# Kernel tuning notes

Hardware: AMD Instinct MI355X
Metric: run time of the kernel (lower is better)

The kernel has to match this reference:

```python
import jax, jax.numpy as jnp
import numpy as np

N, E, G = 50000, 1600000, 512
IN, HID, PROJ = 128, 128, 256


def setup_inputs() -> dict:
    key = jax.random.key(0)
    ks = jax.random.split(key, 20)
    s = 0.05
    return {
        'x1': jax.random.normal(ks[0], (N, IN), jnp.float32),
        'edge_index1': jax.random.randint(ks[1], (2, E), 0, N),
        'batch1': jnp.sort(jax.random.randint(ks[2], (N,), 0, G)),
        'x2': jax.random.normal(ks[3], (N, IN), jnp.float32),
        'edge_index2': jax.random.randint(ks[4], (2, E), 0, N),
        'batch2': jnp.sort(jax.random.randint(ks[5], (N,), 0, G)),
        'W1': jax.random.normal(ks[6], (IN, HID), jnp.float32) * s,
        'b1': jnp.zeros((HID,), jnp.float32),
        'W2': jax.random.normal(ks[7], (HID, HID), jnp.float32) * s,
        'b2': jnp.zeros((HID,), jnp.float32),
        'W3': jax.random.normal(ks[8], (HID, HID), jnp.float32) * s,
        'b3': jnp.zeros((HID,), jnp.float32),
        'Wp1': jax.random.normal(ks[9], (HID, PROJ), jnp.float32) * s,
        'bp1': jnp.zeros((PROJ,), jnp.float32),
        'gamma1': jnp.ones((PROJ,), jnp.float32),
        'beta1': jnp.zeros((PROJ,), jnp.float32),
        'Wp2': jax.random.normal(ks[10], (PROJ, PROJ), jnp.float32) * s,
        'bp2': jnp.zeros((PROJ,), jnp.float32),
        'gamma2': jnp.ones((PROJ,), jnp.float32),
        'beta2': jnp.zeros((PROJ,), jnp.float32),
        'Wq1': jax.random.normal(ks[11], (PROJ, PROJ // 2), jnp.float32) * s,
        'bq1': jnp.zeros((PROJ // 2,), jnp.float32),
        'Wq2': jax.random.normal(ks[12], (PROJ // 2, PROJ), jnp.float32) * s,
        'bq2': jnp.zeros((PROJ,), jnp.float32),
    }


def _gcn_conv(x, src, dst, W, b):
    # PyG GCNConv: add self-loops, symmetric norm, gather -> scatter-add
    n = x.shape[0]
    h = x @ W                                   # [n, out]
    loop = jnp.arange(n)
    s = jnp.concatenate([src, loop])
    d = jnp.concatenate([dst, loop])
    deg = jax.ops.segment_sum(jnp.ones(s.shape[0], h.dtype), d, num_segments=n)
    dinv = jnp.where(deg > 0, 1.0 / jnp.sqrt(deg), 0.0)
    norm = (dinv[s] * dinv[d])[:, None]         # [E+n, 1]
    out = jax.ops.segment_sum(h[s] * norm, d, num_segments=n)
    return out + b


def _encode(x, edge_index, batch, W1, b1, W2, b2, W3, b3):
    src, dst = edge_index[0], edge_index[1]
    h = jax.nn.relu(_gcn_conv(x, src, dst, W1, b1))
    h = jax.nn.relu(_gcn_conv(h, src, dst, W2, b2)) + h
    h = jax.nn.relu(_gcn_conv(h, src, dst, W3, b3)) + h
    # global mean pool over graph ids
    s = jax.ops.segment_sum(h, batch, num_segments=G)
    cnt = jax.ops.segment_sum(jnp.ones(h.shape[0], h.dtype), batch, num_segments=G)
    return s / jnp.maximum(cnt, 1.0)[:, None]


def _batchnorm(x, gamma, beta):
    m = x.mean(axis=0)
    v = x.var(axis=0)  # biased, matches torch BN normalization
    return gamma * (x - m) / jnp.sqrt(v + 1e-5) + beta


def _projector(h, Wp1, bp1, g1, be1, Wp2, bp2, g2, be2):
    z = jax.nn.relu(_batchnorm(h @ Wp1 + bp1, g1, be1))
    return _batchnorm(z @ Wp2 + bp2, g2, be2)


def _predictor(z, Wq1, bq1, Wq2, bq2):
    return jax.nn.relu(z @ Wq1 + bq1) @ Wq2 + bq2


def reference(x1, edge_index1, batch1, x2, edge_index2, batch2,
              W1, b1, W2, b2, W3, b3,
              Wp1, bp1, gamma1, beta1, Wp2, bp2, gamma2, beta2,
              Wq1, bq1, Wq2, bq2):
    h1 = _encode(x1, edge_index1, batch1, W1, b1, W2, b2, W3, b3)
    h2 = _encode(x2, edge_index2, batch2, W1, b1, W2, b2, W3, b3)
    z1 = _projector(h1, Wp1, bp1, gamma1, beta1, Wp2, bp2, gamma2, beta2)
    z2 = _projector(h2, Wp1, bp1, gamma1, beta1, Wp2, bp2, gamma2, beta2)
    p1 = _predictor(z1, Wq1, bq1, Wq2, bq2)
    p2 = _predictor(z2, Wq1, bq1, Wq2, bq2)
    return (p1, p2, z1, z2)
```

## Files before the change

### kernel.cpp

```cpp
#include <hip/hip_runtime.h>
#include <hip/hip_bf16.h>

#define NN     50000
#define NN2    100000
#define NEDGE  1600000
#define NE2    3200000
#define NG     512
#define FIN    128
#define FHID   128
#define FPROJ  256

#define BSH    9
#define BSZ    512
#define NBUCK  98
#define NBUCK2 196
#define EPB    8192
#define NABLK  196
#define NABLK2 392
#define NHIST2 (NBUCK2*NABLK2)
#define NSB1   ((NHIST2 + 255) / 256)

typedef __attribute__((ext_vector_type(8))) short short8;
typedef __attribute__((ext_vector_type(4))) float f32x4;

static __device__ __forceinline__ short f2bf(float f) {
    union { float f; unsigned u; } x; x.f = f;
    unsigned r = (x.u + 0x7FFFu + ((x.u >> 16) & 1u)) >> 16;
    return (short)(r & 0xFFFFu);
}
static __device__ __forceinline__ float bf2f(unsigned short u) {
    union { unsigned u; float f; } x; x.u = ((unsigned)u) << 16;
    return x.f;
}
static __device__ __forceinline__ float bflo(unsigned u) {
    union { unsigned u; float f; } x; x.u = u << 16; return x.f;
}
static __device__ __forceinline__ float bfhi(unsigned u) {
    union { unsigned u; float f; } x; x.u = u & 0xFFFF0000u; return x.f;
}
static __device__ __forceinline__ unsigned packbf(float a, float b) {
    return (unsigned)(unsigned short)f2bf(a) | ((unsigned)(unsigned short)f2bf(b) << 16);
}


__global__ __launch_bounds__(1024) void k_bhist(const int* __restrict__ dst0,
                                                const int* __restrict__ dst1,
                                                int* __restrict__ histG,
                                                unsigned short* __restrict__ lrank) {
    __shared__ int h[NBUCK2];
    for (int j = threadIdx.x; j < NBUCK2; j += 1024) h[j] = 0;
    __syncthreads();
    int b = blockIdx.x;
    int g = b / NABLK, blk = b % NABLK;
    const int* dst = g ? dst1 : dst0;
    int base = blk * EPB;
    int gb = g * NBUCK;
    for (int t = threadIdx.x; t < EPB; t += 1024) {
        int i = base + t;
        if (i < NEDGE)
            lrank[(size_t)g * NEDGE + i] =
                (unsigned short)atomicAdd(&h[gb + (dst[i] >> BSH)], 1);
    }
    __syncthreads();
    for (int j = threadIdx.x; j < NBUCK2; j += 1024)
        histG[(size_t)j * NABLK2 + b] = h[j];
}

__global__ void s_scan256(const int* __restrict__ in, int* __restrict__ out,
                          int* __restrict__ bsum, int n) {
    __shared__ int s[256];
    int i = blockIdx.x * 256 + threadIdx.x;
    int v = (i < n) ? in[i] : 0;
    s[threadIdx.x] = v;
    for (int o = 1; o < 256; o <<= 1) {
        __syncthreads();
        int t = (threadIdx.x >= o) ? s[threadIdx.x - o] : 0;
        __syncthreads();
        s[threadIdx.x] += t;
    }
    __syncthreads();
    if (i < n) out[i] = s[threadIdx.x] - v;
    if (threadIdx.x == 255) bsum[blockIdx.x] = s[255];
}

__global__ __launch_bounds__(512) void s_scan_tail(int* __restrict__ bsum, int nb) {
    __shared__ int s[512];
    int v = (threadIdx.x < nb) ? bsum[threadIdx.x] : 0;
    s[threadIdx.x] = v;
    for (int o = 1; o < 512; o <<= 1) {
        __syncthreads();
        int t = (threadIdx.x >= o) ? s[threadIdx.x - o] : 0;
        __syncthreads();
        s[threadIdx.x] += t;
    }
    __syncthreads();
    if (threadIdx.x < nb) bsum[threadIdx.x] = s[threadIdx.x] - v;
}

__global__ void s_add(int* __restrict__ out, const int* __restrict__ bs, int n) {
    int i = blockIdx.x * 256 + threadIdx.x;
    if (i < n) out[i] += bs[blockIdx.x];
}

__global__ __launch_bounds__(1024) void k_part(const int* __restrict__ src0,
                                               const int* __restrict__ dst0,
                                               const int* __restrict__ src1,
                                               const int* __restrict__ dst1,
                                               const unsigned short* __restrict__ lrank,
                                               const int* __restrict__ histS,
                                               unsigned* __restrict__ pedge) {
    int b = blockIdx.x;
    int g = b / NABLK, blk = b % NABLK;
    const int* src = g ? src1 : src0;
    const int* dst = g ? dst1 : dst0;
    int base = blk * EPB;
    int gb = g * NBUCK;
    for (int t = threadIdx.x; t < EPB; t += 1024) {
        int i = base + t;
        if (i < NEDGE) {
            int d = dst[i];
            int pos = histS[(size_t)(gb + (d >> BSH)) * NABLK2 + b]
                      + (int)lrank[(size_t)g * NEDGE + i];
            pedge[pos] = (unsigned)src[i] | ((unsigned)(d & (BSZ - 1)) << 16);
        }
    }
}

__global__ __launch_bounds__(256) void k_csr(const unsigned* __restrict__ pedge,
                                             const int* __restrict__ histS,
                                             int* __restrict__ csroff,
                                             unsigned short* __restrict__ csrc,
                                             float* __restrict__ dinv) {
    __shared__ int cnt[BSZ], off[BSZ], cur[BSZ];
    int k = blockIdx.x;
    int g = k / NBUCK;
    int nl0 = (k - g * NBUCK) * BSZ;
    int beg = histS[(size_t)k * NABLK2];
    int end = (k == NBUCK2 - 1) ? NE2 : histS[(size_t)(k + 1) * NABLK2];
    for (int t = threadIdx.x; t < BSZ; t += 256) { cnt[t] = 0; cur[t] = 0; }
    __syncthreads();
    for (int e = beg + threadIdx.x; e < end; e += 256)
        atomicAdd(&cnt[(pedge[e] >> 16) & (BSZ - 1)], 1);
    __syncthreads();
    if (threadIdx.x == 0) {
        int s = 0;
        for (int j = 0; j < BSZ; ++j) { off[j] = s; s += cnt[j]; }
    }
    __syncthreads();
    for (int e = beg + threadIdx.x; e < end; e += 256) {
        unsigned v = pedge[e];
        int j = (v >> 16) & (BSZ - 1);
        int r = atomicAdd(&cur[j], 1);
        csrc[beg + off[j] + r] = (unsigned short)(v & 0xFFFFu);
    }
    __syncthreads();
    for (int t = threadIdx.x; t < BSZ; t += 256) {
        int nl = nl0 + t;
        if (nl < NN) {
            int gn = g * NN + nl;
            csroff[gn] = beg + off[t];
            dinv[gn] = 1.0f / sqrtf((float)(cnt[t] + 1));
        }
    }
    if (k == NBUCK2 - 1 && threadIdx.x == 0) csroff[NN2] = NE2;
}


__global__ void k_prepw(const float* __restrict__ W0, const float* __restrict__ W1,
                        const float* __restrict__ W2, short* __restrict__ Wf) {
    int b = blockIdx.x;
    int l = b >> 5; b &= 31;
    const float* W = (l == 0) ? W0 : (l == 1) ? W1 : W2;
    int nt = b >> 2, kt = b & 3;
    int lane = threadIdx.x;
    int n = nt * 16 + (lane & 15);
    int kbase = kt * 32 + (lane >> 4) * 8;
    short8 v;
#pragma unroll
    for (int j = 0; j < 8; ++j) v[j] = f2bf(W[(kbase + j) * FHID + n]);
    *(short8*)(Wf + (size_t)l * 16384 + (size_t)((nt * 4 + kt) * 64 + lane) * 8) = v;
}

__global__ __launch_bounds__(256) void k_gemm(const float* __restrict__ x1,
                                              const float* __restrict__ x2,
                                              const unsigned short* __restrict__ Abf,
                                              const short* __restrict__ Wf,
                                              const float* __restrict__ dinv,
                                              unsigned short* __restrict__ hp) {
    int lane = threadIdx.x & 63;
    int wv = threadIdx.x >> 6;
    int quad = lane >> 4;
    int rowbase = blockIdx.x * 64 + wv * 16;
    int arow = rowbase + (lane & 15);
    if (arow >= NN2) arow = NN2 - 1;

    f32x4 acc[8];
#pragma unroll
    for (int i = 0; i < 8; ++i) acc[i] = (f32x4){0.f, 0.f, 0.f, 0.f};

#pragma unroll
    for (int kt = 0; kt < 4; ++kt) {
        short8 af;
        if (Abf) {
            af = *(const short8*)(Abf + (size_t)arow * FIN + kt * 32 + quad * 8);
        } else {
            const float* ap = (arow < NN ? x1 + (size_t)arow * FIN
                                         : x2 + (size_t)(arow - NN) * FIN)
                              + kt * 32 + quad * 8;
            float4 a0 = *(const float4*)ap;
            float4 a1 = *(const float4*)(ap + 4);
            af[0] = f2bf(a0.x); af[1] = f2bf(a0.y); af[2] = f2bf(a0.z); af[3] = f2bf(a0.w);
            af[4] = f2bf(a1.x); af[5] = f2bf(a1.y); af[6] = f2bf(a1.z); af[7] = f2bf(a1.w);
        }
#pragma unroll
        for (int nt = 0; nt < 8; ++nt) {
            short8 bf = *(const short8*)(Wf + (size_t)((nt * 4 + kt) * 64 + lane) * 8);
            acc[nt] = __builtin_amdgcn_mfma_f32_16x16x32_bf16(af, bf, acc[nt], 0, 0, 0);
        }
    }
    float4 dv = *(const float4*)(dinv + rowbase + quad * 4);
    float dvv[4] = {dv.x, dv.y, dv.z, dv.w};
    int col = lane & 15;
#pragma unroll
    for (int r = 0; r < 4; ++r) {
        int orow = rowbase + quad * 4 + r;
        if (orow < NN2) {
#pragma unroll
            for (int nt = 0; nt < 8; ++nt)
                hp[(size_t)orow * FHID + nt * 16 + col] =
                    (unsigned short)f2bf(acc[nt][r] * dvv[r]);
        }
    }
}


__global__ __launch_bounds__(256) void k_agg(const uint2* __restrict__ hp,
                                             const int* __restrict__ off,
                                             const unsigned short* __restrict__ csrc,
                                             const float* __restrict__ dinv,
                                             const float* __restrict__ bias,
                                             const unsigned short* __restrict__ resid,
                                             unsigned short* __restrict__ hout) {
    int tid = threadIdx.x;
    int l2 = tid & 31;
    int g = blockIdx.x / 6250;
    int lb = blockIdx.x - g * 6250;
    int node = lb * 8 + (tid >> 5);
    size_t nb = (size_t)g * NN;
    const uint2* hpg = hp + nb * 32;
    int gn = (int)nb + node;
    int beg = off[gn], end = off[gn + 1];

    uint2 sv = hpg[(size_t)node * 32 + l2];
    float a0 = bflo(sv.x), a1 = bfhi(sv.x), a2 = bflo(sv.y), a3 = bfhi(sv.y);

    int e = beg;
    for (; e + 16 <= end; e += 16) {
        int s[16];
#pragma unroll
        for (int j = 0; j < 16; ++j) s[j] = (int)csrc[e + j];
        uint2 v[16];
#pragma unroll
        for (int j = 0; j < 16; ++j) v[j] = hpg[(size_t)s[j] * 32 + l2];
#pragma unroll
        for (int j = 0; j < 16; ++j) {
            a0 += bflo(v[j].x); a1 += bfhi(v[j].x);
            a2 += bflo(v[j].y); a3 += bfhi(v[j].y);
        }
    }
    for (; e + 4 <= end; e += 4) {
        int s[4];
#pragma unroll
        for (int j = 0; j < 4; ++j) s[j] = (int)csrc[e + j];
        uint2 v[4];
#pragma unroll
        for (int j = 0; j < 4; ++j) v[j] = hpg[(size_t)s[j] * 32 + l2];
#pragma unroll
        for (int j = 0; j < 4; ++j) {
            a0 += bflo(v[j].x); a1 += bfhi(v[j].x);
            a2 += bflo(v[j].y); a3 += bfhi(v[j].y);
        }
    }
    for (; e < end; ++e) {
        uint2 v = hpg[(size_t)csrc[e] * 32 + l2];
        a0 += bflo(v.x); a1 += bfhi(v.x);
        a2 += bflo(v.y); a3 += bfhi(v.y);
    }
    float dv = dinv[gn];
    float4 b = ((const float4*)bias)[l2];
    float o0 = fmaxf(a0 * dv + b.x, 0.f);
    float o1 = fmaxf(a1 * dv + b.y, 0.f);
    float o2 = fmaxf(a2 * dv + b.z, 0.f);
    float o3 = fmaxf(a3 * dv + b.w, 0.f);
    if (resid) {
        uint2 rv = ((const uint2*)resid)[(size_t)gn * 32 + l2];
        o0 += bflo(rv.x); o1 += bfhi(rv.x);
        o2 += bflo(rv.y); o3 += bfhi(rv.y);
    }
    uint2 ov;
    ov.x = packbf(o0, o1);
    ov.y = packbf(o2, o3);
    ((uint2*)hout)[(size_t)gn * 32 + l2] = ov;
}


static __device__ __forceinline__ int lbound(const int* __restrict__ a, int key) {
    int lo = 0, hi = NN;
    while (lo < hi) { int mid = (lo + hi) >> 1; if (a[mid] < key) lo = mid + 1; else hi = mid; }
    return lo;
}

__global__ void k_pool(const unsigned short* __restrict__ h,
                       const int* __restrict__ b0, const int* __restrict__ b1,
                       float* __restrict__ pooled, float* __restrict__ stats) {
    int b = blockIdx.x;
    int g = b >> 9, lg = b & 511;
    int c = threadIdx.x;
    if (b == 0) {
        for (int i = c; i < 2048; i += 128) stats[i] = 0.f;
    }
    const int* batch = g ? b1 : b0;
    int beg = lbound(batch, lg);
    int end = lbound(batch, lg + 1);
    const unsigned short* hb = h + (size_t)g * NN * FHID;
    float s = 0.f;
    for (int i = beg; i < end; ++i) s += bf2f(hb[(size_t)i * FHID + c]);
    int cnt = end - beg;
    pooled[(size_t)b * FHID + c] = s / (float)(cnt > 0 ? cnt : 1);
}


__global__ void k_mlp(const float* __restrict__ A, const float* __restrict__ W,
                      const float* __restrict__ bias, float* __restrict__ out,
                      int K, int Nc, int act,
                      float* __restrict__ statsOut,
                      const float* __restrict__ statsIn,
                      const float* __restrict__ gIn, const float* __restrict__ beIn) {
    __shared__ float As[8 * 256];
    __shared__ float scl[256], shf[256];
    int n = threadIdx.x;
    int r0 = blockIdx.x * 8;
    int g = blockIdx.x >> 6;
    if (statsIn && n < K) {
        const float* si = statsIn + g * 512;
        float m = si[n] * (1.f / 512.f);
        float var = si[K + n] * (1.f / 512.f) - m * m;
        float inv = 1.0f / sqrtf(var + 1e-5f);
        float s = gIn[n] * inv;
        scl[n] = s;
        shf[n] = beIn[n] - m * s;
    }
    __syncthreads();
    for (int idx = n; idx < 8 * K; idx += blockDim.x) {
        float v = A[(size_t)r0 * K + idx];
        if (statsIn) {
            int k = idx & (K - 1);
            v = fmaxf(v * scl[k] + shf[k], 0.f);
        }
        As[idx] = v;
    }
    __syncthreads();
    float bb = bias[n];
    float acc[8];
#pragma unroll
    for (int r = 0; r < 8; ++r) acc[r] = bb;
    for (int k = 0; k < K; ++k) {
        float w = W[(size_t)k * Nc + n];
#pragma unroll
        for (int r = 0; r < 8; ++r) acc[r] = fmaf(As[r * K + k], w, acc[r]);
    }
    if (statsOut) {
        float s = 0.f, q = 0.f;
#pragma unroll
        for (int r = 0; r < 8; ++r) { s += acc[r]; q += acc[r] * acc[r]; }
        atomicAdd(&statsOut[g * 512 + n], s);
        atomicAdd(&statsOut[g * 512 + Nc + n], q);
    }
#pragma unroll
    for (int r = 0; r < 8; ++r) {
        float v = acc[r];
        if (act) v = fmaxf(v, 0.f);
        out[(size_t)(r0 + r) * Nc + n] = v;
    }
}

__global__ void k_bnapply(const float* __restrict__ X, const float* __restrict__ stats,
                          const float* __restrict__ gamma, const float* __restrict__ beta,
                          float* __restrict__ out, int Nc, int act) {
    int i = blockIdx.x * 256 + threadIdx.x;
    if (i >= 1024 * Nc) return;
    int c = i % Nc;
    int g = i / (512 * Nc);
    const float* st = stats + g * 512;
    float m = st[c] * (1.f / 512.f);
    float var = st[Nc + c] * (1.f / 512.f) - m * m;
    float inv = 1.0f / sqrtf(var + 1e-5f);
    float v = gamma[c] * (X[i] - m) * inv + beta[c];
    if (act) v = fmaxf(v, 0.f);
    out[i] = v;
}


extern "C" void kernel_launch(void* const* d_in, const int* in_sizes, int n_in,
                              void* d_out, int out_size, void* d_ws, size_t ws_size,
                              hipStream_t stream) {
    const float* x1 = (const float*)d_in[0];
    const float* x2 = (const float*)d_in[3];
    const int*   ei[2]    = {(const int*)d_in[1], (const int*)d_in[4]};
    const int*   batch[2] = {(const int*)d_in[2], (const int*)d_in[5]};
    const float* W[3]  = {(const float*)d_in[6], (const float*)d_in[8], (const float*)d_in[10]};
    const float* bb[3] = {(const float*)d_in[7], (const float*)d_in[9], (const float*)d_in[11]};
    const float* Wp1 = (const float*)d_in[12]; const float* bp1 = (const float*)d_in[13];
    const float* g1  = (const float*)d_in[14]; const float* be1 = (const float*)d_in[15];
    const float* Wp2 = (const float*)d_in[16]; const float* bp2 = (const float*)d_in[17];
    const float* g2  = (const float*)d_in[18]; const float* be2 = (const float*)d_in[19];
    const float* Wq1 = (const float*)d_in[20]; const float* bq1 = (const float*)d_in[21];
    const float* Wq2 = (const float*)d_in[22]; const float* bq2 = (const float*)d_in[23];

    char* ws = (char*)d_ws;
    size_t off = 0;
    auto alloc = [&](size_t bytes) -> void* {
        void* p = ws + off;
        off += (bytes + 255) & ~(size_t)255;
        return p;
    };
    unsigned short* h_cur  = (unsigned short*)alloc((size_t)NN2 * FHID * 2);
    unsigned short* hp     = (unsigned short*)alloc((size_t)NN2 * FHID * 2);
    unsigned short* csrc   = (unsigned short*)alloc((size_t)NE2 * 2);
    int*            csroff = (int*)alloc((size_t)(NN2 + 1) * 4);
    unsigned short* lrank  = (unsigned short*)alloc((size_t)NE2 * 2);
    unsigned*       pedge  = (unsigned*)alloc((size_t)NE2 * 4);
    int*            histG  = (int*)alloc((size_t)NHIST2 * 4);
    int*            histS  = (int*)alloc((size_t)NHIST2 * 4);
    int*            bsum   = (int*)alloc(512 * 4);
    float*          dinv   = (float*)alloc((size_t)100352 * 4);
    float*          pooled = (float*)alloc((size_t)2 * NG * FHID * 4);
    short*          Wf     = (short*)alloc((size_t)3 * 16384 * 2);
    float*          t1     = (float*)alloc((size_t)1024 * 256 * 4);
    float*          t2     = (float*)alloc((size_t)1024 * 256 * 4);
    float*          t3     = (float*)alloc((size_t)1024 * 128 * 4);
    float*          stats  = (float*)alloc(2048 * 4);

    const int* src0 = ei[0];           const int* dst0 = ei[0] + NEDGE;
    const int* src1 = ei[1];           const int* dst1 = ei[1] + NEDGE;

    k_prepw<<<96, 64, 0, stream>>>(W[0], W[1], W[2], Wf);

    k_bhist<<<NABLK2, 1024, 0, stream>>>(dst0, dst1, histG, lrank);
    s_scan256<<<NSB1, 256, 0, stream>>>(histG, histS, bsum, NHIST2);
    s_scan_tail<<<1, 512, 0, stream>>>(bsum, NSB1);
    s_add<<<NSB1, 256, 0, stream>>>(histS, bsum, NHIST2);
    k_part<<<NABLK2, 1024, 0, stream>>>(src0, dst0, src1, dst1, lrank, histS, pedge);
    k_csr<<<NBUCK2, 256, 0, stream>>>(pedge, histS, csroff, csrc, dinv);

    for (int l = 0; l < 3; ++l) {
        const unsigned short* Abf = (l == 0) ? nullptr : h_cur;
        const unsigned short* resid = (l == 0) ? nullptr : h_cur;
        k_gemm<<<1564, 256, 0, stream>>>(x1, x2, Abf, Wf + (size_t)l * 16384, dinv, hp);
        k_agg<<<12500, 256, 0, stream>>>((const uint2*)hp, csroff, csrc, dinv,
                                         bb[l], resid, h_cur);
    }
    k_pool<<<1024, 128, 0, stream>>>(h_cur, batch[0], batch[1], pooled, stats);

    float* outp = (float*)d_out;
    float* p_out = outp;
    float* z_out = outp + (size_t)2 * NG * FPROJ;
    float* st1 = stats, *st2 = stats + 1024;
    k_mlp<<<128, 256, 0, stream>>>(pooled, Wp1, bp1, t1,
                                   128, 256, 0, st1, nullptr, nullptr, nullptr);
    k_mlp<<<128, 256, 0, stream>>>(t1, Wp2, bp2, t2,
                                   256, 256, 0, st2, st1, g1, be1);
    k_bnapply<<<1024, 256, 0, stream>>>(t2, st2, g2, be2, z_out, 256, 0);
    k_mlp<<<128, 128, 0, stream>>>(z_out, Wq1, bq1, t3,
                                   256, 128, 1, nullptr, nullptr, nullptr, nullptr);
    k_mlp<<<128, 256, 0, stream>>>(t3, Wq2, bq2, p_out,
                                   128, 256, 0, nullptr, nullptr, nullptr, nullptr);
}
```

Baseline: 737.5 us.

## Split GCN aggregation by feature quarter and edge sub-range with shuffle reduction

The aggregation kernel now launches four times as many blocks. Each block handles one quarter of the feature columns, and each node's 32 lanes are split into 4 groups of 8 lanes. Each group sums a contiguous quarter of the node's edge list, and the partial sums are combined with cross-lane xor shuffles. Edge indices and the residual are read with nontemporal loads, the output is written with a nontemporal store, and bf16 unpacking uses a float2 vector helper. The aim is more memory-level parallelism per node and shorter dependent chains. In exchange, each gathered row is fetched in 64-byte pieces by separate blocks and the CSR index array is read four times.

```diff
diff --git a/kernel.cpp b/kernel.cpp
--- a/kernel.cpp
+++ b/kernel.cpp
@@ -20,8 +20,12 @@
 #define NHIST2 (NBUCK2*NABLK2)
 #define NSB1   ((NHIST2 + 255) / 256)
 
+#define AGG_BPP 6250
+
 typedef __attribute__((ext_vector_type(8))) short short8;
 typedef __attribute__((ext_vector_type(4))) float f32x4;
+typedef __attribute__((ext_vector_type(2))) float f32x2;
+typedef __attribute__((ext_vector_type(2))) unsigned u32x2;
 
 static __device__ __forceinline__ short f2bf(float f) {
     union { float f; unsigned u; } x; x.f = f;
@@ -40,6 +44,12 @@
 }
 static __device__ __forceinline__ unsigned packbf(float a, float b) {
     return (unsigned)(unsigned short)f2bf(a) | ((unsigned)(unsigned short)f2bf(b) << 16);
+}
+static __device__ __forceinline__ f32x2 bfpair(unsigned u) {
+    union { unsigned v[2]; f32x2 f; } x;
+    x.v[0] = u << 16;
+    x.v[1] = u & 0xFFFF0000u;
+    return x.f;
 }
 
 
@@ -234,7 +244,7 @@
 }
 
 
-__global__ __launch_bounds__(256) void k_agg(const uint2* __restrict__ hp,
+__global__ __launch_bounds__(256) void k_agg(const u32x2* __restrict__ hp,
                                              const int* __restrict__ off,
                                              const unsigned short* __restrict__ csrc,
                                              const float* __restrict__ dinv,
@@ -242,65 +252,79 @@
                                              const unsigned short* __restrict__ resid,
                                              unsigned short* __restrict__ hout) {
     int tid = threadIdx.x;
-    int l2 = tid & 31;
-    int g = blockIdx.x / 6250;
-    int lb = blockIdx.x - g * 6250;
-    int node = lb * 8 + (tid >> 5);
+    int nodeL = tid >> 5;
+    int l32 = tid & 31;
+    int grp = l32 >> 3;
+    int l8 = l32 & 7;
+    int p  = blockIdx.x / AGG_BPP;
+    int lb = blockIdx.x - p * AGG_BPP;
+    int g  = p & 1;
+    int q  = p >> 1;
+    int idx = q * 8 + l8;
+    int node = lb * 8 + nodeL;
     size_t nb = (size_t)g * NN;
-    const uint2* hpg = hp + nb * 32;
+    const u32x2* hpg = hp + nb * 32;
     int gn = (int)nb + node;
     int beg = off[gn], end = off[gn + 1];
-
-    uint2 sv = hpg[(size_t)node * 32 + l2];
-    float a0 = bflo(sv.x), a1 = bfhi(sv.x), a2 = bflo(sv.y), a3 = bfhi(sv.y);
-
-    int e = beg;
-    for (; e + 16 <= end; e += 16) {
-        int s[16];
-#pragma unroll
-        for (int j = 0; j < 16; ++j) s[j] = (int)csrc[e + j];
-        uint2 v[16];
-#pragma unroll
-        for (int j = 0; j < 16; ++j) v[j] = hpg[(size_t)s[j] * 32 + l2];
-#pragma unroll
-        for (int j = 0; j < 16; ++j) {
-            a0 += bflo(v[j].x); a1 += bfhi(v[j].x);
-            a2 += bflo(v[j].y); a3 += bfhi(v[j].y);
-        }
-    }
-    for (; e + 4 <= end; e += 4) {
-        int s[4];
-#pragma unroll
-        for (int j = 0; j < 4; ++j) s[j] = (int)csrc[e + j];
-        uint2 v[4];
-#pragma unroll
-        for (int j = 0; j < 4; ++j) v[j] = hpg[(size_t)s[j] * 32 + l2];
-#pragma unroll
-        for (int j = 0; j < 4; ++j) {
-            a0 += bflo(v[j].x); a1 += bfhi(v[j].x);
-            a2 += bflo(v[j].y); a3 += bfhi(v[j].y);
-        }
-    }
-    for (; e < end; ++e) {
-        uint2 v = hpg[(size_t)csrc[e] * 32 + l2];
-        a0 += bflo(v.x); a1 += bfhi(v.x);
-        a2 += bflo(v.y); a3 += bfhi(v.y);
-    }
-    float dv = dinv[gn];
-    float4 b = ((const float4*)bias)[l2];
-    float o0 = fmaxf(a0 * dv + b.x, 0.f);
-    float o1 = fmaxf(a1 * dv + b.y, 0.f);
-    float o2 = fmaxf(a2 * dv + b.z, 0.f);
-    float o3 = fmaxf(a3 * dv + b.w, 0.f);
-    if (resid) {
-        uint2 rv = ((const uint2*)resid)[(size_t)gn * 32 + l2];
-        o0 += bflo(rv.x); o1 += bfhi(rv.x);
-        o2 += bflo(rv.y); o3 += bfhi(rv.y);
-    }
-    uint2 ov;
-    ov.x = packbf(o0, o1);
-    ov.y = packbf(o2, o3);
-    ((uint2*)hout)[(size_t)gn * 32 + l2] = ov;
+    int cnt = end - beg;
+    int len = (cnt + 3) >> 2;
+    int gb = beg + grp * len;
+    int ge = gb + len; if (ge > end) ge = end;
+
+    f32x2 a01 = (f32x2){0.f, 0.f}, a23 = (f32x2){0.f, 0.f};
+    if (grp == 0) {
+        u32x2 sv = hpg[(size_t)node * 32 + idx];
+        a01 += bfpair(sv.x); a23 += bfpair(sv.y);
+    }
+
+    int e = gb;
+    for (; e + 8 <= ge; e += 8) {
+        int s[8];
+#pragma unroll
+        for (int j = 0; j < 8; ++j)
+            s[j] = (int)__builtin_nontemporal_load(&csrc[e + j]);
+        u32x2 v[8];
+#pragma unroll
+        for (int j = 0; j < 8; ++j) v[j] = hpg[(size_t)s[j] * 32 + idx];
+#pragma unroll
+        for (int j = 0; j < 8; ++j) { a01 += bfpair(v[j].x); a23 += bfpair(v[j].y); }
+    }
+    for (; e + 2 <= ge; e += 2) {
+        int s0 = (int)__builtin_nontemporal_load(&csrc[e]);
+        int s1 = (int)__builtin_nontemporal_load(&csrc[e + 1]);
+        u32x2 v0 = hpg[(size_t)s0 * 32 + idx];
+        u32x2 v1 = hpg[(size_t)s1 * 32 + idx];
+        a01 += bfpair(v0.x); a23 += bfpair(v0.y);
+        a01 += bfpair(v1.x); a23 += bfpair(v1.y);
+    }
+    for (; e < ge; ++e) {
+        u32x2 v = hpg[(size_t)__builtin_nontemporal_load(&csrc[e]) * 32 + idx];
+        a01 += bfpair(v.x); a23 += bfpair(v.y);
+    }
+
+    a01.x += __shfl_xor(a01.x, 8);  a01.y += __shfl_xor(a01.y, 8);
+    a23.x += __shfl_xor(a23.x, 8);  a23.y += __shfl_xor(a23.y, 8);
+    a01.x += __shfl_xor(a01.x, 16); a01.y += __shfl_xor(a01.y, 16);
+    a23.x += __shfl_xor(a23.x, 16); a23.y += __shfl_xor(a23.y, 16);
+
+    if (l32 < 8) {
+        float dv = dinv[gn];
+        float4 b = ((const float4*)bias)[idx];
+        float o0 = fmaxf(a01.x * dv + b.x, 0.f);
+        float o1 = fmaxf(a01.y * dv + b.y, 0.f);
+        float o2 = fmaxf(a23.x * dv + b.z, 0.f);
+        float o3 = fmaxf(a23.y * dv + b.w, 0.f);
+        if (resid) {
+            u32x2 rv = __builtin_nontemporal_load(
+                &((const u32x2*)resid)[(size_t)gn * 32 + idx]);
+            o0 += bflo(rv.x); o1 += bfhi(rv.x);
+            o2 += bflo(rv.y); o3 += bfhi(rv.y);
+        }
+        u32x2 ov;
+        ov.x = packbf(o0, o1);
+        ov.y = packbf(o2, o3);
+        __builtin_nontemporal_store(ov, &((u32x2*)hout)[(size_t)gn * 32 + idx]);
+    }
 }
 
 
@@ -457,8 +481,8 @@
         const unsigned short* Abf = (l == 0) ? nullptr : h_cur;
         const unsigned short* resid = (l == 0) ? nullptr : h_cur;
         k_gemm<<<1564, 256, 0, stream>>>(x1, x2, Abf, Wf + (size_t)l * 16384, dinv, hp);
-        k_agg<<<12500, 256, 0, stream>>>((const uint2*)hp, csroff, csrc, dinv,
-                                         bb[l], resid, h_cur);
+        k_agg<<<8 * AGG_BPP, 256, 0, stream>>>((const u32x2*)hp, csroff, csrc, dinv,
+                                               bb[l], resid, h_cur);
     }
     k_pool<<<1024, 128, 0, stream>>>(h_cur, batch[0], batch[1], pooled, stats);
 
```

After: 1.040 ms. +41.0%, slower.
